# Performance work log

Hardware: AMD Instinct MI355X
Metric: run time of the kernel (lower is better)

The kernel has to match this reference:

```python
import jax, jax.numpy as jnp
import numpy as np

N, B, L, E = 64, 128, 4096, 16
BN_EPS = 1e-5


def setup_inputs() -> dict:
    key = jax.random.key(0)
    ks = jax.random.split(key, 6)
    feat = jax.random.normal(ks[0], (N, B, L), dtype=jnp.float32)
    # Glorot-ish scaled linear weights
    Wl = jax.random.normal(ks[1], (L, E), dtype=jnp.float32) * (1.0 / np.sqrt(L))
    Wr = jax.random.normal(ks[2], (L, E), dtype=jnp.float32) * (1.0 / np.sqrt(L))
    Wm = jax.random.normal(ks[3], (L, L), dtype=jnp.float32) * (1.0 / np.sqrt(L))
    return {
        "feat": feat,
        "Wl": Wl, "bl": jnp.zeros((E,), jnp.float32),
        "Wr": Wr, "br": jnp.zeros((E,), jnp.float32),
        "Wm": Wm, "bm": jnp.zeros((L,), jnp.float32),
        "gamma": jnp.ones((N * N,), jnp.float32),
        "beta": jnp.zeros((N * N,), jnp.float32),
        "bias": jnp.zeros((L,), jnp.float32),
    }


def reference(feat, Wl, bl, Wr, br, Wm, bm, gamma, beta, bias):
    # feat: (N, B, L) node time series
    # Attention projections (lookup_l / lookup_r): Linear(L -> E)
    att_l = feat @ Wl + bl                      # (N, B, E) on src nodes
    att_r = feat @ Wr + br                      # (N, B, E) on dst nodes

    # Feature extractor: MLP Linear(L, L) + ReLU over the time axis
    out = jax.nn.relu(jnp.einsum('nbl,kl->nbk', feat, Wm) + bm)   # (N, B, L)

    # Edge scores on the complete graph: e[d, s, b] = att_l[src=s] . att_r[dst=d]
    e = jnp.einsum('sbe,dbe->dsb', att_l, att_r)                  # (Nd, Ns, B)

    # BatchNorm1d over N*N edge channels (training-mode batch statistics)
    ef = e.reshape(N * N, B)
    mu = ef.mean(axis=1, keepdims=True)
    var = ef.var(axis=1, keepdims=True)
    ef = gamma[:, None] * (ef - mu) * jax.lax.rsqrt(var + BN_EPS) + beta[:, None]
    e = ef.reshape(N, N, B)

    # edge_softmax: normalize over incoming edges (src axis) per destination node
    w = jax.nn.softmax(e, axis=1)                                  # (Nd, Ns, B)

    # Weighted neighbor aggregation + bias
    rst = jnp.einsum('dsb,sbl->dbl', w, out) + bias                # (N, B, L)
    return rst
```

## Files before the change

### kernel.cpp

```cpp
#include <hip/hip_runtime.h>
#include <stdint.h>
#include <stddef.h>

#define NN 64
#define BB 128
#define LL 4096
#define EE 16

typedef __attribute__((ext_vector_type(4))) float f32x4;
typedef __attribute__((ext_vector_type(2))) float f32x2;
typedef __attribute__((ext_vector_type(8))) short short8;
typedef __attribute__((ext_vector_type(4))) unsigned short u16x4;

__device__ __forceinline__ unsigned short f2bf(float f) {
  union { float f; unsigned u; } v; v.f = f;
  unsigned r = v.u + 0x7FFFu + ((v.u >> 16) & 1u);
  return (unsigned short)(r >> 16);
}
__device__ __forceinline__ float bf2f(unsigned short h) {
  union { unsigned u; float f; } v; v.u = ((unsigned)h) << 16;
  return v.f;
}
__device__ __forceinline__ void gload16(const void* g, void* l) {
  __builtin_amdgcn_global_load_lds((const __attribute__((address_space(1))) void*)g,
                                   (__attribute__((address_space(3))) void*)l,
                                   16, 0, 0);
}

__global__ __launch_bounds__(256) void k_cvtw(const float* __restrict__ Wm,
    const float* __restrict__ Wl, const float* __restrict__ Wr,
    unsigned short* __restrict__ wm_bf, unsigned short* __restrict__ wt_bf) {
  int bid = blockIdx.x;
  if (bid < 2048) {
    int i = bid * 256 + threadIdx.x;
    for (; i < (LL * LL / 4); i += 2048 * 256) {
      f32x4 v = ((const f32x4*)Wm)[i];
      u16x4 o;
      o[0] = f2bf(v[0]); o[1] = f2bf(v[1]); o[2] = f2bf(v[2]); o[3] = f2bf(v[3]);
      ((u16x4*)wm_bf)[i] = o;
    }
  } else {
    int u = (bid - 2048) * 256 + threadIdx.x;
    int e = u >> 6;
    int kb = (u & 63) * 64;
    const float* src = (e < 16) ? (Wl + e) : (Wr + (e - 16));
    for (int k = kb; k < kb + 64; ++k)
      wt_bf[(size_t)e * LL + k] = f2bf(src[(size_t)k * 16]);
  }
}

__global__ __launch_bounds__(256) void k_cvtf(const float* __restrict__ feat,
                                              unsigned short* __restrict__ feat_bf) {
  int i = blockIdx.x * 256 + threadIdx.x;
  const int n4 = NN * BB * LL / 4;
  for (; i < n4; i += 2048 * 256) {
    f32x4 v = ((const f32x4*)feat)[i];
    u16x4 o;
    o[0] = f2bf(v[0]); o[1] = f2bf(v[1]); o[2] = f2bf(v[2]); o[3] = f2bf(v[3]);
    ((u16x4*)feat_bf)[i] = o;
  }
}

#define MFMA(a, b, c) __builtin_amdgcn_mfma_f32_16x16x32_bf16((a), (b), (c), 0, 0, 0)

__global__ __launch_bounds__(256) void k_attm(const unsigned short* __restrict__ feat_bf,
    const unsigned short* __restrict__ wt_bf, float* __restrict__ attP) {
  const int t = threadIdx.x, lane = t & 63, w = t >> 6;
  const int rowTile = blockIdx.x;
  const int kc = blockIdx.y;
  const int grow = rowTile * 64 + w * 16 + (lane & 15);
  const int kbase = kc * 1024 + (lane >> 4) * 8;
  const unsigned short* aP  = feat_bf + (size_t)grow * LL + kbase;
  const unsigned short* b0P = wt_bf + (size_t)(lane & 15) * LL + kbase;
  const unsigned short* b1P = wt_bf + (size_t)(16 + (lane & 15)) * LL + kbase;
  f32x4 acc0 = {}, acc1 = {};
  #pragma unroll 4
  for (int ks = 0; ks < 32; ++ks) {
    short8 av = *(const short8*)(aP + ks * 32);
    short8 b0 = *(const short8*)(b0P + ks * 32);
    short8 b1 = *(const short8*)(b1P + ks * 32);
    acc0 = MFMA(av, b0, acc0);
    acc1 = MFMA(av, b1, acc1);
  }
  const int orow = rowTile * 64 + w * 16 + (lane >> 4) * 4;
  const int col = lane & 15;
  float* P = attP + (size_t)kc * (8192 * 32);
  #pragma unroll
  for (int j = 0; j < 4; ++j) {
    P[(size_t)(orow + j) * 32 + col]      = acc0[j];
    P[(size_t)(orow + j) * 32 + 16 + col] = acc1[j];
  }
}

__global__ __launch_bounds__(256) void k_edge(const float* __restrict__ attP,
    const float* __restrict__ bl, const float* __restrict__ br,
    const float* __restrict__ gamma, const float* __restrict__ beta,
    float* __restrict__ w_t) {
  __shared__ __align__(16) float attr[BB][20];
  __shared__ float el[NN][BB + 1];
  __shared__ float part[NN][4][2];
  __shared__ float sc[NN], sh[NN];
  int d = blockIdx.x, t = threadIdx.x;
  for (int i = t; i < 2048; i += 256) {
    int b = i >> 4, e = i & 15;
    float v2 = br[e];
    #pragma unroll
    for (int c = 0; c < 4; ++c)
      v2 += attP[(size_t)c * (8192 * 32) + ((size_t)d * 128 + b) * 32 + 16 + e];
    attr[b][e] = v2;
  }
  float blv[16];
  #pragma unroll
  for (int e = 0; e < 16; ++e) blv[e] = bl[e];
  __syncthreads();
  for (int v = t; v < NN * BB; v += 256) {
    int s = v >> 7, b = v & 127;
    float al[16];
    #pragma unroll
    for (int e = 0; e < 16; ++e) al[e] = blv[e];
    #pragma unroll
    for (int c = 0; c < 4; ++c) {
      const f32x4* p = (const f32x4*)&attP[(size_t)c * (8192 * 32) + ((size_t)s * 128 + b) * 32];
      #pragma unroll
      for (int q = 0; q < 4; ++q) {
        f32x4 x = p[q];
        al[q * 4 + 0] += x[0]; al[q * 4 + 1] += x[1];
        al[q * 4 + 2] += x[2]; al[q * 4 + 3] += x[3];
      }
    }
    float acc = 0.f;
    #pragma unroll
    for (int e = 0; e < 16; ++e) acc += al[e] * attr[b][e];
    el[s][b] = acc;
  }
  __syncthreads();
  {
    int s = t >> 2, q = t & 3;
    float sum = 0.f, ss = 0.f;
    for (int b = q * 32; b < q * 32 + 32; ++b) { float x = el[s][b]; sum += x; ss += x * x; }
    part[s][q][0] = sum; part[s][q][1] = ss;
  }
  __syncthreads();
  if (t < 64) {
    float sum = 0.f, ss = 0.f;
    #pragma unroll
    for (int q = 0; q < 4; ++q) { sum += part[t][q][0]; ss += part[t][q][1]; }
    float mu = sum * (1.f / 128.f);
    float var = ss * (1.f / 128.f) - mu * mu;
    int c = d * 64 + t;
    float a = gamma[c] * rsqrtf(fmaxf(var, 0.f) + 1e-5f);
    sc[t] = a; sh[t] = beta[c] - mu * a;
  }
  __syncthreads();
  if (t < 128) {
    int b = t;
    float y[64];
    float m = -1e30f;
    #pragma unroll
    for (int s = 0; s < 64; ++s) { y[s] = sc[s] * el[s][b] + sh[s]; m = fmaxf(m, y[s]); }
    float sum = 0.f;
    #pragma unroll
    for (int s = 0; s < 64; ++s) { y[s] = __expf(y[s] - m); sum += y[s]; }
    float inv = 1.f / sum;
    float* wp = &w_t[((size_t)b * 64 + d) * 64];
    #pragma unroll
    for (int s4 = 0; s4 < 16; ++s4) {
      f32x4 o;
      o[0] = y[s4 * 4 + 0] * inv; o[1] = y[s4 * 4 + 1] * inv;
      o[2] = y[s4 * 4 + 2] * inv; o[3] = y[s4 * 4 + 3] * inv;
      *(f32x4*)&wp[s4 * 4] = o;
    }
  }
}

#define LDS_A 0
#define LDS_B 65536
#define BAR   __builtin_amdgcn_s_barrier()
#define VM6   asm volatile("s_waitcnt vmcnt(6)" ::: "memory")
#define VM4   asm volatile("s_waitcnt vmcnt(4)" ::: "memory")
#define VM0   asm volatile("s_waitcnt vmcnt(0)" ::: "memory")
#define PRIO1 __builtin_amdgcn_s_setprio(1)
#define PRIO0 __builtin_amdgcn_s_setprio(0)
#define STAGE2(g0, g1, ldsoff) do { \
    gload16((g0), lds_raw + (ldsoff) + tid16); \
    gload16((g1), lds_raw + (ldsoff) + 8192 + tid16); } while (0)

__global__ __launch_bounds__(512, 2) void k_gemm8(const unsigned short* __restrict__ A,
    const unsigned short* __restrict__ Bm, const float* __restrict__ bm,
    unsigned short* __restrict__ C) {
  __shared__ __align__(16) char lds_raw[131072];
  const int tid = threadIdx.x;
  const int lane = tid & 63, wave = tid >> 6;
  const int wm = wave >> 2, wn = wave & 3;
  int bid = blockIdx.x;
  int swz = (bid & 7) * 64 + (bid >> 3);
  int tM = swz >> 4, tN = swz & 15;
  const size_t rowBase = (size_t)tM * 256, colBase = (size_t)tN * 256;
  const int tid16 = tid * 16;
  const int o0 = tid16, o1 = tid16 + 8192;
  const int r0s = (o0 & 1023) >> 6, r1s = (o1 & 1023) >> 6;
  const int row0 = (o0 >> 10) * 16 + r0s, row1 = (o1 >> 10) * 16 + r1s;
  const int col0 = (((o0 >> 4) & 3) ^ ((r0s >> 3) << 1)) * 8;
  const int col1 = (((o1 >> 4) & 3) ^ ((r1s >> 3) << 1)) * 8;
  const unsigned short* aR0 = A  + (rowBase + row0) * LL + col0;
  const unsigned short* aR1 = A  + (rowBase + row1) * LL + col1;
  const unsigned short* bR0 = Bm + (colBase + row0) * LL + col0;
  const unsigned short* bR1 = Bm + (colBase + row1) * LL + col1;
  const int rr = lane & 15, gg = lane >> 4;
  const int rdswz = rr * 64 + ((gg ^ ((rr >> 3) << 1)) << 4);
  f32x4 acc[8][4] = {};
  STAGE2(aR0 +  0, aR1 +  0, LDS_A + 0);
  STAGE2(bR0 +  0, bR1 +  0, LDS_B + 0);
  STAGE2(aR0 + 32, aR1 + 32, LDS_A + 16384);
  STAGE2(bR0 + 32, bR1 + 32, LDS_B + 16384);
  VM4;
  STAGE2(aR0 + 64, aR1 + 64, LDS_A + 32768);
  STAGE2(bR0 + 64, bR1 + 64, LDS_B + 32768);
  STAGE2(aR0 + 96, aR1 + 96, LDS_A + 32768 + 16384);
  VM6;
  BAR;
  #pragma unroll 2
  for (int t = 0; t < 64; ++t) {
    const int d = t & 1;
    const char* pA = lds_raw + LDS_A + d * 32768 + wm * 8192 + rdswz;
    const char* pB = lds_raw + LDS_B + d * 32768 + wn * 4096 + rdswz;
    short8 ar[8], bx, by;
    bx = *(const short8*)(pB + 0);
    by = *(const short8*)(pB + 1024);
    #pragma unroll
    for (int mi = 0; mi < 8; ++mi) ar[mi] = *(const short8*)(pA + mi * 1024);
    if (t <= 62) { size_t kc = (size_t)(t + 1) * 64 + 32;
      STAGE2(bR0 + kc, bR1 + kc, LDS_B + ((t + 1) & 1) * 32768 + 16384); }
    BAR; PRIO1;
    #pragma unroll
    for (int mi = 0; mi < 8; ++mi) {
      acc[mi][0] = MFMA(ar[mi], bx, acc[mi][0]);
      acc[mi][1] = MFMA(ar[mi], by, acc[mi][1]);
    }
    PRIO0; BAR;
    bx = *(const short8*)(pB + 2048);
    by = *(const short8*)(pB + 3072);
    if (t <= 61) { size_t kc = (size_t)(t + 2) * 64;
      STAGE2(aR0 + kc, aR1 + kc, LDS_A + d * 32768); }
    BAR; PRIO1;
    #pragma unroll
    for (int mi = 0; mi < 8; ++mi) {
      acc[mi][2] = MFMA(ar[mi], bx, acc[mi][2]);
      acc[mi][3] = MFMA(ar[mi], by, acc[mi][3]);
    }
    PRIO0; BAR;
    bx = *(const short8*)(pB + 16384 + 2048);
    by = *(const short8*)(pB + 16384 + 3072);
    #pragma unroll
    for (int mi = 0; mi < 8; ++mi) ar[mi] = *(const short8*)(pA + 16384 + mi * 1024);
    if (t <= 61) { size_t kc = (size_t)(t + 2) * 64;
      STAGE2(bR0 + kc, bR1 + kc, LDS_B + d * 32768); }
    BAR; PRIO1;
    #pragma unroll
    for (int mi = 0; mi < 8; ++mi) {
      acc[mi][2] = MFMA(ar[mi], bx, acc[mi][2]);
      acc[mi][3] = MFMA(ar[mi], by, acc[mi][3]);
    }
    PRIO0; BAR;
    bx = *(const short8*)(pB + 16384);
    by = *(const short8*)(pB + 16384 + 1024);
    if (t <= 61) { size_t kc = (size_t)(t + 2) * 64 + 32;
      STAGE2(aR0 + kc, aR1 + kc, LDS_A + d * 32768 + 16384); }
    BAR; PRIO1;
    #pragma unroll
    for (int mi = 0; mi < 8; ++mi) {
      acc[mi][0] = MFMA(ar[mi], bx, acc[mi][0]);
      acc[mi][1] = MFMA(ar[mi], by, acc[mi][1]);
    }
    PRIO0;
    if (t < 62) { VM6; } else { VM0; }
    BAR;
  }
  const int co = lane & 15, ro4 = (lane >> 4) * 4;
  #pragma unroll
  for (int mig = 0; mig < 8; ++mig) {
    size_t r0 = rowBase + (size_t)wm * 128 + mig * 16 + ro4;
    #pragma unroll
    for (int nj = 0; nj < 4; ++nj) {
      size_t c = colBase + (size_t)wn * 64 + nj * 16 + co;
      float bc = bm[c];
      #pragma unroll
      for (int j = 0; j < 4; ++j) {
        float v = acc[mig][nj][j] + bc;
        v = fmaxf(v, 0.f);
        C[(r0 + j) * LL + c] = f2bf(v);
      }
    }
  }
}

__global__ __launch_bounds__(256) void k_agg2(const float* __restrict__ w_t,
    const unsigned short* __restrict__ outb, const float* __restrict__ bias,
    float* __restrict__ rst) {
  int b = blockIdx.y;
  int t = threadIdx.x;
  int l0 = blockIdx.x * 512 + t * 2;
  float oA[64], oB[64];
  #pragma unroll
  for (int s = 0; s < 64; ++s) {
    unsigned u = *(const unsigned*)&outb[((size_t)s * BB + b) * LL + l0];
    oA[s] = bf2f((unsigned short)(u & 0xFFFF));
    oB[s] = bf2f((unsigned short)(u >> 16));
  }
  const float* wb = w_t + (size_t)b * 4096;
  float bs0 = bias[l0], bs1 = bias[l0 + 1];
  #pragma unroll 2
  for (int d = 0; d < 64; ++d) {
    const float* wr = wb + d * 64;
    float a0 = 0.f, a1 = 0.f;
    #pragma unroll
    for (int q = 0; q < 16; ++q) {
      f32x4 wq = *(const f32x4*)&wr[q * 4];
      #pragma unroll
      for (int j = 0; j < 4; ++j) {
        float wv = wq[j];
        a0 += wv * oA[q * 4 + j];
        a1 += wv * oB[q * 4 + j];
      }
    }
    f32x2 o; o[0] = a0 + bs0; o[1] = a1 + bs1;
    *(f32x2*)&rst[((size_t)d * BB + b) * LL + l0] = o;
  }
}

extern "C" void kernel_launch(void* const* d_in, const int* in_sizes, int n_in,
                              void* d_out, int out_size, void* d_ws, size_t ws_size,
                              hipStream_t stream) {
  (void)in_sizes; (void)n_in; (void)out_size; (void)ws_size;
  const float* feat  = (const float*)d_in[0];
  const float* Wl    = (const float*)d_in[1];
  const float* bl    = (const float*)d_in[2];
  const float* Wr    = (const float*)d_in[3];
  const float* br    = (const float*)d_in[4];
  const float* Wm    = (const float*)d_in[5];
  const float* bm    = (const float*)d_in[6];
  const float* gamma = (const float*)d_in[7];
  const float* beta  = (const float*)d_in[8];
  const float* bias  = (const float*)d_in[9];
  char* ws = (char*)d_ws;
  unsigned short* feat_bf = (unsigned short*)(ws);
  unsigned short* wm_bf   = (unsigned short*)(ws + 67108864ull);
  unsigned short* out_bf  = (unsigned short*)(ws + 100663296ull);
  float* attP  = (float*)(ws + 167772160ull);
  float* w_t   = (float*)(ws + 171966464ull);
  unsigned short* wt_bf = (unsigned short*)(ws + 174063616ull);
  float* rst = (float*)d_out;

  k_cvtw<<<dim3(2056), dim3(256), 0, stream>>>(Wm, Wl, Wr, wm_bf, wt_bf);
  k_cvtf<<<dim3(2048), dim3(256), 0, stream>>>(feat, feat_bf);
  k_attm<<<dim3(128, 4), dim3(256), 0, stream>>>(feat_bf, wt_bf, attP);
  k_edge<<<dim3(64), dim3(256), 0, stream>>>(attP, bl, br, gamma, beta, w_t);
  k_gemm8<<<dim3(512), dim3(512), 0, stream>>>(feat_bf, wm_bf, bm, out_bf);
  k_agg2<<<dim3(8, 128), dim3(256), 0, stream>>>(w_t, out_bf, bias, rst);
}
```

Before: 478.1 us.

## Fuse feat bf16 conversion into attention projection and restructure GEMM pipeline

Merges the separate fp32-to-bf16 conversion of feat into the attention projection kernel. That kernel now converts tiles into LDS, writes the bf16 copy out, and feeds MFMAs from the staged tile, which removes one full read of the bf16 feat. The K split is halved from 4 to 2, and the edge kernel's partial-sum reduction is updated to match. Separately, the main GEMM inner loop is rescheduled into 4x4 MFMA sub-blocks with a different prefetch order and waitcnt depths, aiming for better register reuse and overlap. The attention kernel now has only 256 blocks with serialized staging, which risks low occupancy and poor latency hiding.

New measurement: 442.3 us. -7.5%, faster.

```diff
diff --git a/kernel.cpp b/kernel.cpp
--- a/kernel.cpp
+++ b/kernel.cpp
@@ -26,6 +26,8 @@
                                    (__attribute__((address_space(3))) void*)l,
                                    16, 0, 0);
 }
+
+#define MFMA(a, b, c) __builtin_amdgcn_mfma_f32_16x16x32_bf16((a), (b), (c), 0, 0, 0)
 
 __global__ __launch_bounds__(256) void k_cvtw(const float* __restrict__ Wm,
     const float* __restrict__ Wl, const float* __restrict__ Wr,
@@ -49,46 +51,51 @@
   }
 }
 
-__global__ __launch_bounds__(256) void k_cvtf(const float* __restrict__ feat,
-                                              unsigned short* __restrict__ feat_bf) {
-  int i = blockIdx.x * 256 + threadIdx.x;
-  const int n4 = NN * BB * LL / 4;
-  for (; i < n4; i += 2048 * 256) {
-    f32x4 v = ((const f32x4*)feat)[i];
-    u16x4 o;
-    o[0] = f2bf(v[0]); o[1] = f2bf(v[1]); o[2] = f2bf(v[2]); o[3] = f2bf(v[3]);
-    ((u16x4*)feat_bf)[i] = o;
-  }
-}
-
-#define MFMA(a, b, c) __builtin_amdgcn_mfma_f32_16x16x32_bf16((a), (b), (c), 0, 0, 0)
-
-__global__ __launch_bounds__(256) void k_attm(const unsigned short* __restrict__ feat_bf,
-    const unsigned short* __restrict__ wt_bf, float* __restrict__ attP) {
+__global__ __launch_bounds__(256) void k_attF(const float* __restrict__ feat,
+    const unsigned short* __restrict__ wt_bf,
+    unsigned short* __restrict__ feat_bf, float* __restrict__ attP) {
+  __shared__ __align__(16) unsigned short alds[64 * 512];
   const int t = threadIdx.x, lane = t & 63, w = t >> 6;
-  const int rowTile = blockIdx.x;
-  const int kc = blockIdx.y;
-  const int grow = rowTile * 64 + w * 16 + (lane & 15);
-  const int kbase = kc * 1024 + (lane >> 4) * 8;
-  const unsigned short* aP  = feat_bf + (size_t)grow * LL + kbase;
-  const unsigned short* b0P = wt_bf + (size_t)(lane & 15) * LL + kbase;
-  const unsigned short* b1P = wt_bf + (size_t)(16 + (lane & 15)) * LL + kbase;
+  const int rowBase = blockIdx.x * 64;
+  const int kBase = blockIdx.y * 2048;
+  const int rr = lane & 15, gg8 = (lane >> 4) * 8;
   f32x4 acc0 = {}, acc1 = {};
-  #pragma unroll 4
-  for (int ks = 0; ks < 32; ++ks) {
-    short8 av = *(const short8*)(aP + ks * 32);
-    short8 b0 = *(const short8*)(b0P + ks * 32);
-    short8 b1 = *(const short8*)(b1P + ks * 32);
-    acc0 = MFMA(av, b0, acc0);
-    acc1 = MFMA(av, b1, acc1);
-  }
-  const int orow = rowTile * 64 + w * 16 + (lane >> 4) * 4;
-  const int col = lane & 15;
-  float* P = attP + (size_t)kc * (8192 * 32);
+  const unsigned short* b0P = wt_bf + (size_t)rr * LL;
+  const unsigned short* b1P = wt_bf + (size_t)(16 + rr) * LL;
+  for (int c = 0; c < 4; ++c) {
+    const int k0 = kBase + c * 512;
+    __syncthreads();
+    #pragma unroll
+    for (int u = 0; u < 32; ++u) {
+      int unit = t + u * 256;
+      int row = unit >> 7, col4 = unit & 127;
+      size_t gi = (size_t)(rowBase + row) * LL + k0 + col4 * 4;
+      f32x4 v = *(const f32x4*)&feat[gi];
+      u16x4 o; o[0] = f2bf(v[0]); o[1] = f2bf(v[1]); o[2] = f2bf(v[2]); o[3] = f2bf(v[3]);
+      *(u16x4*)&feat_bf[gi] = o;
+      int byte = (row * 1024 + col4 * 8) ^ ((row & 7) << 4);
+      *(u16x4*)((char*)alds + byte) = o;
+    }
+    __syncthreads();
+    const int arow = w * 16 + rr;
+    const char* aBase = (const char*)alds + arow * 1024;
+    const int axor = (arow & 7) << 4;
+    #pragma unroll 4
+    for (int ks = 0; ks < 16; ++ks) {
+      int abyte = ((ks * 32 + gg8) * 2) ^ axor;
+      short8 av = *(const short8*)(aBase + abyte);
+      short8 b0 = *(const short8*)(b0P + k0 + ks * 32 + gg8);
+      short8 b1 = *(const short8*)(b1P + k0 + ks * 32 + gg8);
+      acc0 = MFMA(av, b0, acc0);
+      acc1 = MFMA(av, b1, acc1);
+    }
+  }
+  const int orow = rowBase + w * 16 + (lane >> 4) * 4;
+  float* P = attP + (size_t)blockIdx.y * (8192 * 32);
   #pragma unroll
   for (int j = 0; j < 4; ++j) {
-    P[(size_t)(orow + j) * 32 + col]      = acc0[j];
-    P[(size_t)(orow + j) * 32 + 16 + col] = acc1[j];
+    P[(size_t)(orow + j) * 32 + rr]      = acc0[j];
+    P[(size_t)(orow + j) * 32 + 16 + rr] = acc1[j];
   }
 }
 
@@ -105,7 +112,7 @@
     int b = i >> 4, e = i & 15;
     float v2 = br[e];
     #pragma unroll
-    for (int c = 0; c < 4; ++c)
+    for (int c = 0; c < 2; ++c)
       v2 += attP[(size_t)c * (8192 * 32) + ((size_t)d * 128 + b) * 32 + 16 + e];
     attr[b][e] = v2;
   }
@@ -119,7 +126,7 @@
     #pragma unroll
     for (int e = 0; e < 16; ++e) al[e] = blv[e];
     #pragma unroll
-    for (int c = 0; c < 4; ++c) {
+    for (int c = 0; c < 2; ++c) {
       const f32x4* p = (const f32x4*)&attP[(size_t)c * (8192 * 32) + ((size_t)s * 128 + b) * 32];
       #pragma unroll
       for (int q = 0; q < 4; ++q) {
@@ -176,8 +183,9 @@
 #define LDS_A 0
 #define LDS_B 65536
 #define BAR   __builtin_amdgcn_s_barrier()
-#define VM6   asm volatile("s_waitcnt vmcnt(6)" ::: "memory")
+#define VM8   asm volatile("s_waitcnt vmcnt(8)" ::: "memory")
 #define VM4   asm volatile("s_waitcnt vmcnt(4)" ::: "memory")
+#define VM2   asm volatile("s_waitcnt vmcnt(2)" ::: "memory")
 #define VM0   asm volatile("s_waitcnt vmcnt(0)" ::: "memory")
 #define PRIO1 __builtin_amdgcn_s_setprio(1)
 #define PRIO0 __builtin_amdgcn_s_setprio(0)
@@ -213,69 +221,78 @@
   STAGE2(bR0 +  0, bR1 +  0, LDS_B + 0);
   STAGE2(aR0 + 32, aR1 + 32, LDS_A + 16384);
   STAGE2(bR0 + 32, bR1 + 32, LDS_B + 16384);
-  VM4;
+  STAGE2(bR0 + 64, bR1 + 64, LDS_B + 32768);
   STAGE2(aR0 + 64, aR1 + 64, LDS_A + 32768);
-  STAGE2(bR0 + 64, bR1 + 64, LDS_B + 32768);
-  STAGE2(aR0 + 96, aR1 + 96, LDS_A + 32768 + 16384);
-  VM6;
+  VM8;
   BAR;
   #pragma unroll 2
   for (int t = 0; t < 64; ++t) {
     const int d = t & 1;
     const char* pA = lds_raw + LDS_A + d * 32768 + wm * 8192 + rdswz;
     const char* pB = lds_raw + LDS_B + d * 32768 + wn * 4096 + rdswz;
-    short8 ar[8], bx, by;
-    bx = *(const short8*)(pB + 0);
-    by = *(const short8*)(pB + 1024);
-    #pragma unroll
-    for (int mi = 0; mi < 8; ++mi) ar[mi] = *(const short8*)(pA + mi * 1024);
-    if (t <= 62) { size_t kc = (size_t)(t + 1) * 64 + 32;
-      STAGE2(bR0 + kc, bR1 + kc, LDS_B + ((t + 1) & 1) * 32768 + 16384); }
+    short8 ar[4], bf4[4];
+    #pragma unroll
+    for (int i = 0; i < 4; ++i) bf4[i] = *(const short8*)(pB + i * 1024);
+    #pragma unroll
+    for (int i = 0; i < 4; ++i) ar[i] = *(const short8*)(pA + i * 1024);
+    if (t <= 62) { size_t kk = (size_t)(t + 1) * 64 + 32;
+      STAGE2(aR0 + kk, aR1 + kk, LDS_A + ((t + 1) & 1) * 32768 + 16384); }
     BAR; PRIO1;
     #pragma unroll
-    for (int mi = 0; mi < 8; ++mi) {
-      acc[mi][0] = MFMA(ar[mi], bx, acc[mi][0]);
-      acc[mi][1] = MFMA(ar[mi], by, acc[mi][1]);
+    for (int i = 0; i < 4; ++i) {
+      acc[i][0] = MFMA(ar[i], bf4[0], acc[i][0]);
+      acc[i][1] = MFMA(ar[i], bf4[1], acc[i][1]);
+      acc[i][2] = MFMA(ar[i], bf4[2], acc[i][2]);
+      acc[i][3] = MFMA(ar[i], bf4[3], acc[i][3]);
     }
     PRIO0; BAR;
-    bx = *(const short8*)(pB + 2048);
-    by = *(const short8*)(pB + 3072);
-    if (t <= 61) { size_t kc = (size_t)(t + 2) * 64;
-      STAGE2(aR0 + kc, aR1 + kc, LDS_A + d * 32768); }
+    #pragma unroll
+    for (int i = 0; i < 4; ++i) ar[i] = *(const short8*)(pA + 4096 + i * 1024);
+    if (t <= 61) { size_t kk = (size_t)(t + 2) * 64;
+      STAGE2(bR0 + kk, bR1 + kk, LDS_B + d * 32768); }
     BAR; PRIO1;
     #pragma unroll
-    for (int mi = 0; mi < 8; ++mi) {
-      acc[mi][2] = MFMA(ar[mi], bx, acc[mi][2]);
-      acc[mi][3] = MFMA(ar[mi], by, acc[mi][3]);
+    for (int i = 0; i < 4; ++i) {
+      acc[4 + i][0] = MFMA(ar[i], bf4[0], acc[4 + i][0]);
+      acc[4 + i][1] = MFMA(ar[i], bf4[1], acc[4 + i][1]);
+      acc[4 + i][2] = MFMA(ar[i], bf4[2], acc[4 + i][2]);
+      acc[4 + i][3] = MFMA(ar[i], bf4[3], acc[4 + i][3]);
+    }
+    PRIO0;
+    if (t <= 61) { VM4; } else if (t == 62) { VM2; } else { VM0; }
+    BAR;
+    #pragma unroll
+    for (int i = 0; i < 4; ++i) bf4[i] = *(const short8*)(pB + 16384 + i * 1024);
+    #pragma unroll
+    for (int i = 0; i < 4; ++i) ar[i] = *(const short8*)(pA + 16384 + i * 1024);
+    if (t <= 61) { size_t kk = (size_t)(t + 2) * 64;
+      STAGE2(aR0 + kk, aR1 + kk, LDS_A + d * 32768); }
+    BAR; PRIO1;
+    #pragma unroll
+    for (int i = 0; i < 4; ++i) {
+      acc[i][0] = MFMA(ar[i], bf4[0], acc[i][0]);
+      acc[i][1] = MFMA(ar[i], bf4[1], acc[i][1]);
+      acc[i][2] = MFMA(ar[i], bf4[2], acc[i][2]);
+      acc[i][3] = MFMA(ar[i], bf4[3], acc[i][3]);
     }
     PRIO0; BAR;
-    bx = *(const short8*)(pB + 16384 + 2048);
-    by = *(const short8*)(pB + 16384 + 3072);
-    #pragma unroll
-    for (int mi = 0; mi < 8; ++mi) ar[mi] = *(const short8*)(pA + 16384 + mi * 1024);
-    if (t <= 61) { size_t kc = (size_t)(t + 2) * 64;
-      STAGE2(bR0 + kc, bR1 + kc, LDS_B + d * 32768); }
+    #pragma unroll
+    for (int i = 0; i < 4; ++i) ar[i] = *(const short8*)(pA + 16384 + 4096 + i * 1024);
+    if (t <= 62) { size_t kk = (size_t)(t + 1) * 64 + 32;
+      STAGE2(bR0 + kk, bR1 + kk, LDS_B + ((t + 1) & 1) * 32768 + 16384); }
     BAR; PRIO1;
     #pragma unroll
-    for (int mi = 0; mi < 8; ++mi) {
-      acc[mi][2] = MFMA(ar[mi], bx, acc[mi][2]);
-      acc[mi][3] = MFMA(ar[mi], by, acc[mi][3]);
-    }
-    PRIO0; BAR;
-    bx = *(const short8*)(pB + 16384);
-    by = *(const short8*)(pB + 16384 + 1024);
-    if (t <= 61) { size_t kc = (size_t)(t + 2) * 64 + 32;
-      STAGE2(aR0 + kc, aR1 + kc, LDS_A + d * 32768 + 16384); }
-    BAR; PRIO1;
-    #pragma unroll
-    for (int mi = 0; mi < 8; ++mi) {
-      acc[mi][0] = MFMA(ar[mi], bx, acc[mi][0]);
-      acc[mi][1] = MFMA(ar[mi], by, acc[mi][1]);
+    for (int i = 0; i < 4; ++i) {
+      acc[4 + i][0] = MFMA(ar[i], bf4[0], acc[4 + i][0]);
+      acc[4 + i][1] = MFMA(ar[i], bf4[1], acc[4 + i][1]);
+      acc[4 + i][2] = MFMA(ar[i], bf4[2], acc[4 + i][2]);
+      acc[4 + i][3] = MFMA(ar[i], bf4[3], acc[4 + i][3]);
     }
     PRIO0;
-    if (t < 62) { VM6; } else { VM0; }
+    if (t <= 61) { VM8; } else { VM4; }
     BAR;
   }
+  VM0;
   const int co = lane & 15, ro4 = (lane >> 4) * 4;
   #pragma unroll
   for (int mig = 0; mig < 8; ++mig) {
@@ -347,13 +364,12 @@
   unsigned short* wm_bf   = (unsigned short*)(ws + 67108864ull);
   unsigned short* out_bf  = (unsigned short*)(ws + 100663296ull);
   float* attP  = (float*)(ws + 167772160ull);
-  float* w_t   = (float*)(ws + 171966464ull);
-  unsigned short* wt_bf = (unsigned short*)(ws + 174063616ull);
+  float* w_t   = (float*)(ws + 169869312ull);
+  unsigned short* wt_bf = (unsigned short*)(ws + 171966464ull);
   float* rst = (float*)d_out;
 
   k_cvtw<<<dim3(2056), dim3(256), 0, stream>>>(Wm, Wl, Wr, wm_bf, wt_bf);
-  k_cvtf<<<dim3(2048), dim3(256), 0, stream>>>(feat, feat_bf);
-  k_attm<<<dim3(128, 4), dim3(256), 0, stream>>>(feat_bf, wt_bf, attP);
+  k_attF<<<dim3(128, 2), dim3(256), 0, stream>>>(feat, wt_bf, feat_bf, attP);
   k_edge<<<dim3(64), dim3(256), 0, stream>>>(attP, bl, br, gamma, beta, w_t);
   k_gemm8<<<dim3(512), dim3(512), 0, stream>>>(feat_bf, wm_bf, bm, out_bf);
   k_agg2<<<dim3(8, 128), dim3(256), 0, stream>>>(w_t, out_bf, bias, rst);
```
